# Performance work log

Measured on AMD Instinct MI355X. Metric: run time of the kernel, lower is better.

Reference implementation:

```python
import jax, jax.numpy as jnp
import numpy as np

EMBED = 1024
HEADS = 16
HEAD_DIM = EMBED // HEADS


def setup_inputs() -> dict:
    key = jax.random.key(0)
    ks = jax.random.split(key, 9)
    s = 1.0 / np.sqrt(EMBED)
    return {
        "x": jax.random.normal(ks[0], (4, 1024, EMBED), dtype=jnp.float32),
        "wq": jax.random.normal(ks[1], (EMBED, EMBED), dtype=jnp.float32) * s,
        "bq": jax.random.normal(ks[2], (EMBED,), dtype=jnp.float32) * s,
        "wk": jax.random.normal(ks[3], (EMBED, EMBED), dtype=jnp.float32) * s,
        "bk": jax.random.normal(ks[4], (EMBED,), dtype=jnp.float32) * s,
        "wv": jax.random.normal(ks[5], (EMBED, EMBED), dtype=jnp.float32) * s,
        "bv": jax.random.normal(ks[6], (EMBED,), dtype=jnp.float32) * s,
        "wo": jax.random.normal(ks[7], (EMBED, EMBED), dtype=jnp.float32) * s,
        "bo": jax.random.normal(ks[8], (EMBED,), dtype=jnp.float32) * s,
    }


def _split_heads(t):
    # (b, s, e) -> (b, h, s, d)
    b, s, _ = t.shape
    return t.reshape(b, s, HEADS, HEAD_DIM).transpose(0, 2, 1, 3)


def reference(x, wq, bq, wk, bk, wv, bv, wo, bo):
    # nn.Linear: y = x @ W.T + b
    q = _split_heads(x @ wq.T + bq)
    k = _split_heads(x @ wk.T + bk)
    v = _split_heads(x @ wv.T + bv)
    scale = 1.0 / jnp.sqrt(jnp.asarray(HEAD_DIM, dtype=x.dtype))
    scores = jnp.einsum("bhqd,bhkd->bhqk", q, k) * scale
    attn = jax.nn.softmax(scores, axis=-1)  # (b, h, s, s)
    ctx = jnp.einsum("bhqk,bhkd->bhqd", attn, v)
    b, h, s, d = ctx.shape
    ctx = ctx.transpose(0, 2, 1, 3).reshape(b, s, h * d)
    out = ctx @ wo.T + bo
    return out, attn
```

## Files before the change

kernel.cpp:

```cpp
#include <hip/hip_runtime.h>
#include <math.h>

#define BATCH 4
#define SEQ   1024
#define EMB   1024
#define HEADS 16
#define HD    64
#define MTOT  (BATCH*SEQ)

typedef float    f32x4 __attribute__((ext_vector_type(4)));
typedef float    vf4   __attribute__((ext_vector_type(4)));
typedef _Float16 f16;
typedef _Float16 f16x4 __attribute__((ext_vector_type(4)));
typedef _Float16 f16x8 __attribute__((ext_vector_type(8)));

__global__ __launch_bounds__(256) void convert_all(
    const float* __restrict__ x,
    const float* __restrict__ wq, const float* __restrict__ wk,
    const float* __restrict__ wv, const float* __restrict__ wo,
    f16* __restrict__ xh, f16* __restrict__ wh)
{
    const int bid = blockIdx.x;
    const float* src;
    f16* dst;
    if (bid < 4096) {
        src = x + ((size_t)bid << 10);
        dst = xh + ((size_t)bid << 10);
    } else {
        int t  = bid - 4096;
        int mi = t >> 10, r = t & 1023;
        const float* in = (mi == 0) ? wq : (mi == 1) ? wk : (mi == 2) ? wv : wo;
        src = in + ((size_t)r << 10);
        dst = wh + ((size_t)mi << 20) + ((size_t)r << 10);
    }
    int o = threadIdx.x << 2;
    float4 v = *(const float4*)(src + o);
    f16x4 h;
    h.x = (f16)v.x; h.y = (f16)v.y; h.z = (f16)v.z; h.w = (f16)v.w;
    *(f16x4*)(dst + o) = h;
}

#define BM  128
#define BN  128
#define LDT 72

__device__ __forceinline__ void mfma_gemm_tile(
    const f16* __restrict__ A, const f16* __restrict__ B,
    int m0, int n0, f32x4 acc[4][4])
{
    __shared__ f16 As[BM * LDT];
    __shared__ f16 Bs[BM * LDT];
    const int tid  = threadIdx.x;
    const int lane = tid & 63;
    const int w    = tid >> 6;
    const int wr   = w >> 1, wc = w & 1;
    const int fr   = lane & 15;
    const int kb   = lane >> 4;

#pragma unroll
    for (int i = 0; i < 4; ++i)
#pragma unroll
        for (int j = 0; j < 4; ++j) acc[i][j] = (f32x4){0.f, 0.f, 0.f, 0.f};

    f16x8 ra[4], rb[4];
#define LOAD_STEP(KT)                                                          \
    {                                                                          \
        int k0 = (KT) * 64;                                                    \
        _Pragma("unroll")                                                      \
        for (int i = 0; i < 4; ++i) {                                          \
            int c = tid + (i << 8);                                            \
            int row = c >> 3, cc = (c & 7) << 3;                               \
            ra[i] = *(const f16x8*)(A + ((size_t)(m0 + row) << 10) + k0 + cc); \
            rb[i] = *(const f16x8*)(B + ((size_t)(n0 + row) << 10) + k0 + cc); \
        }                                                                      \
    }

    LOAD_STEP(0);
    for (int kt = 0; kt < 16; ++kt) {
        __syncthreads();
#pragma unroll
        for (int i = 0; i < 4; ++i) {
            int c = tid + (i << 8);
            int row = c >> 3, cc = (c & 7) << 3;
            *(f16x8*)&As[row * LDT + cc] = ra[i];
            *(f16x8*)&Bs[row * LDT + cc] = rb[i];
        }
        if (kt + 1 < 16) LOAD_STEP(kt + 1);
        __syncthreads();
#pragma unroll
        for (int kc = 0; kc < 2; ++kc) {
            f16x8 aF[4], bF[4];
#pragma unroll
            for (int i = 0; i < 4; ++i)
                aF[i] = *(const f16x8*)&As[(wr * 64 + i * 16 + fr) * LDT + kc * 32 + kb * 8];
#pragma unroll
            for (int j = 0; j < 4; ++j)
                bF[j] = *(const f16x8*)&Bs[(wc * 64 + j * 16 + fr) * LDT + kc * 32 + kb * 8];
#pragma unroll
            for (int i = 0; i < 4; ++i)
#pragma unroll
                for (int j = 0; j < 4; ++j)
                    acc[i][j] = __builtin_amdgcn_mfma_f32_16x16x32_f16(
                        aF[i], bF[j], acc[i][j], 0, 0, 0);
        }
    }
#undef LOAD_STEP
}

__global__ __launch_bounds__(256, 2) void qkv_mfma(
    const f16* __restrict__ xh, const f16* __restrict__ wh,
    const float* __restrict__ bq, const float* __restrict__ bk,
    const float* __restrict__ bv,
    f16* __restrict__ qh, f16* __restrict__ kh, f16* __restrict__ vth)
{
    const int z = blockIdx.z;
    const f16* Bm = wh + ((size_t)z << 20);
    const float* bias = (z == 0) ? bq : (z == 1) ? bk : bv;
    const int m0 = blockIdx.y * BM, n0 = blockIdx.x * BN;
    f32x4 acc[4][4];
    mfma_gemm_tile(xh, Bm, m0, n0, acc);

    const int lane = threadIdx.x & 63;
    const int w    = threadIdx.x >> 6;
    const int wr   = w >> 1, wc = w & 1;
    const int fr   = lane & 15;
    const int rg   = lane >> 4;
#pragma unroll
    for (int i = 0; i < 4; ++i)
#pragma unroll
        for (int j = 0; j < 4; ++j) {
            int n = n0 + wc * 64 + j * 16 + fr;
            int h = n >> 6, d = n & 63;
            float bv_ = bias[n];
            int m_base = m0 + wr * 64 + i * 16 + rg * 4;
            int b = m_base >> 10, s0 = m_base & 1023;
            if (z < 2) {
                f16* p = (z == 0) ? qh : kh;
#pragma unroll
                for (int r = 0; r < 4; ++r) {
                    float v = acc[i][j][r] + bv_;
                    p[((size_t)((b * HEADS + h) * SEQ + s0 + r)) * HD + d] = (f16)v;
                }
            } else {
                f16x4 h4;
                h4.x = (f16)(acc[i][j][0] + bv_);
                h4.y = (f16)(acc[i][j][1] + bv_);
                h4.z = (f16)(acc[i][j][2] + bv_);
                h4.w = (f16)(acc[i][j][3] + bv_);
                size_t a = ((size_t)((b * HEADS + h) * HD + d)) * SEQ + s0;
                *(f16x4*)(vth + a) = h4;
            }
        }
}

__global__ __launch_bounds__(256, 2) void oproj_mfma(
    const f16* __restrict__ ch, const f16* __restrict__ wh,
    const float* __restrict__ bo, float* __restrict__ out)
{
    const f16* Bm = wh + ((size_t)3 << 20);
    const int m0 = blockIdx.y * BM, n0 = blockIdx.x * BN;
    f32x4 acc[4][4];
    mfma_gemm_tile(ch, Bm, m0, n0, acc);

    const int lane = threadIdx.x & 63;
    const int w    = threadIdx.x >> 6;
    const int wr   = w >> 1, wc = w & 1;
    const int fr   = lane & 15;
    const int rg   = lane >> 4;
#pragma unroll
    for (int i = 0; i < 4; ++i)
#pragma unroll
        for (int j = 0; j < 4; ++j) {
            int n = n0 + wc * 64 + j * 16 + fr;
            float bv_ = bo[n];
#pragma unroll
            for (int r = 0; r < 4; ++r) {
                int m = m0 + wr * 64 + i * 16 + rg * 4 + r;
                out[(size_t)m * EMB + n] = acc[i][j][r] + bv_;
            }
        }
}

__global__ __launch_bounds__(512, 4) void attn_kernel(
    const f16* __restrict__ qh, const f16* __restrict__ kh,
    const f16* __restrict__ vth,
    float* __restrict__ attn, f16* __restrict__ ch)
{
    __shared__ f16 SM[12288];
    __shared__ float RMAX[8][16];
    __shared__ float RSUM[8][16];

    const int lid = blockIdx.y * gridDim.x + blockIdx.x;
    const int xs  = lid & 7;
    const int jj  = lid >> 3;
    const int bh  = xs * 8 + (jj >> 5);
    const int qt  = jj & 31;

    const int tid  = threadIdx.x;
    const int w    = tid >> 6;
    const int grp  = w >> 2;
    const int wg   = w & 3;
    const int lane = tid & 63;
    const int c    = lane & 15;
    const int g    = lane >> 4;

    const size_t bhS = (size_t)bh * SEQ;

    f16x8 Q0, Q1;
    {
        size_t qb = (bhS + qt * 32 + grp * 16 + c) * HD + g * 8;
        Q0 = *(const f16x8*)(qh + qb);
        Q1 = *(const f16x8*)(qh + qb + 32);
    }

    f32x4 s4[16];
#pragma unroll
    for (int kt = 0; kt < 16; ++kt) s4[kt] = (f32x4){0.f, 0.f, 0.f, 0.f};

    const int srow = tid >> 3;
    const int sch  = tid & 7;
    const int sswz = sch ^ (srow & 7);
#pragma unroll
    for (int kt = 0; kt < 16; ++kt) {
        size_t ga = (bhS + kt * 64 + srow) * HD + sch * 8;
        f16x8 sh = *(const f16x8*)(kh + ga);
        __syncthreads();
        *(f16x8*)&SM[srow * 64 + sswz * 8] = sh;
        __syncthreads();
        const int krow = wg * 16 + c;
        const int cs   = c & 7;
        f16x8 B0 = *(const f16x8*)&SM[krow * 64 + ((0 + g) ^ cs) * 8];
        f16x8 B1 = *(const f16x8*)&SM[krow * 64 + ((4 + g) ^ cs) * 8];
        s4[kt] = __builtin_amdgcn_mfma_f32_16x16x32_f16(Q0, B0, s4[kt], 0, 0, 0);
        s4[kt] = __builtin_amdgcn_mfma_f32_16x16x32_f16(Q1, B1, s4[kt], 0, 0, 0);
    }

    float m_[4], l_[4];
#pragma unroll
    for (int r = 0; r < 4; ++r) {
        float mm = -1e30f;
#pragma unroll
        for (int kt = 0; kt < 16; ++kt) {
            s4[kt][r] *= 0.125f;
            mm = fmaxf(mm, s4[kt][r]);
        }
        m_[r] = mm;
    }
#pragma unroll
    for (int off = 1; off < 16; off <<= 1)
#pragma unroll
        for (int r = 0; r < 4; ++r) m_[r] = fmaxf(m_[r], __shfl_xor(m_[r], off));
    if (c == 0) {
#pragma unroll
        for (int r = 0; r < 4; ++r) RMAX[w][g * 4 + r] = m_[r];
    }
    __syncthreads();
#pragma unroll
    for (int r = 0; r < 4; ++r)
        m_[r] = fmaxf(fmaxf(RMAX[grp * 4 + 0][g * 4 + r], RMAX[grp * 4 + 1][g * 4 + r]),
                      fmaxf(RMAX[grp * 4 + 2][g * 4 + r], RMAX[grp * 4 + 3][g * 4 + r]));
#pragma unroll
    for (int r = 0; r < 4; ++r) {
        float ss = 0.f;
#pragma unroll
        for (int kt = 0; kt < 16; ++kt) {
            float p = __expf(s4[kt][r] - m_[r]);
            s4[kt][r] = p;
            ss += p;
        }
        l_[r] = ss;
    }
#pragma unroll
    for (int off = 1; off < 16; off <<= 1)
#pragma unroll
        for (int r = 0; r < 4; ++r) l_[r] += __shfl_xor(l_[r], off);
    if (c == 0) {
#pragma unroll
        for (int r = 0; r < 4; ++r) RSUM[w][g * 4 + r] = l_[r];
    }
    __syncthreads();
#pragma unroll
    for (int r = 0; r < 4; ++r)
        l_[r] = 1.f / (RSUM[grp * 4 + 0][g * 4 + r] + RSUM[grp * 4 + 1][g * 4 + r] +
                       RSUM[grp * 4 + 2][g * 4 + r] + RSUM[grp * 4 + 3][g * 4 + r]);

    f32x4 ctx = (f32x4){0.f, 0.f, 0.f, 0.f};
    float* ap = attn + (bhS + qt * 32) * SEQ;
    const int vrow0 = tid >> 4;
    const int vch   = tid & 15;

#pragma unroll
    for (int ct = 0; ct < 8; ++ct) {
        f16x8 vv[2];
#pragma unroll
        for (int t = 0; t < 2; ++t) {
            int drow = vrow0 + t * 32;
            size_t ga = ((size_t)bh * HD + drow) * SEQ + ct * 128 + vch * 8;
            vv[t] = *(const f16x8*)(vth + ga);
        }
        __syncthreads();
#pragma unroll
        for (int t = 0; t < 2; ++t) {
            int drow = vrow0 + t * 32;
            int swz = vch ^ (drow & 7);
            *(f16x8*)&SM[drow * 128 + swz * 8] = vv[t];
        }
#pragma unroll
        for (int kt2 = 0; kt2 < 2; ++kt2) {
            const int ktg = ct * 2 + kt2;
            const int chh = (kt2 * 64 + wg * 16 + c) >> 3;
#pragma unroll
            for (int r = 0; r < 4; ++r) {
                const int q = g * 4 + r;
                float val = s4[ktg][r] * l_[r];
                int schP = chh ^ q;
                SM[8192 + (grp * 16 + q) * 128 + schP * 8 + (c & 7)] = (f16)val;
            }
        }
        __syncthreads();
        const int drow = wg * 16 + c;
        const int ds7  = drow & 7;
#pragma unroll
        for (int ks = 0; ks < 4; ++ks) {
            f16x8 Vh = *(const f16x8*)&SM[drow * 128 + ((ks * 4 + g) ^ ds7) * 8];
            f16x8 Pa = *(const f16x8*)&SM[8192 + (grp * 16 + c) * 128 + (((ks * 4 + g) ^ c) & 15) * 8];
            ctx = __builtin_amdgcn_mfma_f32_16x16x32_f16(Pa, Vh, ctx, 0, 0, 0);
        }
#pragma unroll
        for (int t = 0; t < 2; ++t) {
            int idx = tid + (t << 9);
            int row = idx >> 5;
            int c4  = idx & 31;
            int col = c4 << 2;
            int swz = (col >> 3) ^ (row & 15);
            f16x4 pv = *(const f16x4*)&SM[8192 + row * 128 + swz * 8 + (col & 7)];
            vf4 o = __builtin_convertvector(pv, vf4);
            __builtin_nontemporal_store(o,
                (vf4*)(ap + (size_t)row * SEQ + ct * 128 + col));
        }
    }

    {
        int b = bh >> 4, h = bh & 15;
#pragma unroll
        for (int r = 0; r < 4; ++r) {
            int qrow = qt * 32 + grp * 16 + g * 4 + r;
            size_t a = (((size_t)(b * SEQ + qrow)) << 10) + h * HD + wg * 16 + c;
            ch[a] = (f16)ctx[r];
        }
    }
}

extern "C" void kernel_launch(void* const* d_in, const int* in_sizes, int n_in,
                              void* d_out, int out_size, void* d_ws, size_t ws_size,
                              hipStream_t stream) {
    const float* x  = (const float*)d_in[0];
    const float* wq = (const float*)d_in[1];
    const float* bq = (const float*)d_in[2];
    const float* wk = (const float*)d_in[3];
    const float* bk = (const float*)d_in[4];
    const float* wv = (const float*)d_in[5];
    const float* bv = (const float*)d_in[6];
    const float* wo = (const float*)d_in[7];
    const float* bo = (const float*)d_in[8];

    float* out      = (float*)d_out;
    float* attn_out = out + (size_t)BATCH * SEQ * EMB;

    const size_t MK = (size_t)MTOT * 1024;
    f16* ws16 = (f16*)d_ws;
    f16* xh  = ws16;
    f16* wh  = xh + MK;
    f16* qh  = wh + ((size_t)4 << 20);
    f16* kh  = qh + MK;
    f16* vth = kh + MK;
    f16* ch  = xh;

    convert_all<<<8192, 256, 0, stream>>>(x, wq, wk, wv, wo, xh, wh);

    qkv_mfma<<<dim3(EMB / BN, MTOT / BM, 3), 256, 0, stream>>>(
        xh, wh, bq, bk, bv, qh, kh, vth);

    attn_kernel<<<dim3(SEQ / 32, BATCH * HEADS), 512, 0, stream>>>(
        qh, kh, vth, attn_out, ch);

    oproj_mfma<<<dim3(EMB / BN, MTOT / BM), 256, 0, stream>>>(
        ch, wh, bo, out);
}
```

Before: 148.2 us.

## Stage GEMM epilogues through LDS and prefetch K/V tiles in attention

The QKV and output-projection GEMM epilogues now write through shared memory so global stores go out as coalesced 16-byte vectors, replacing scattered 2-byte and 4-byte stores. This includes the transposed V layout. The attention kernel loads K in 128-row chunks and prefetches the next K and V tile into registers while the current tile is staged and consumed. This hides global load latency and halves the barrier pairs in the QK loop. In exchange it adds extra LDS round trips and barriers in the epilogues and raises register pressure in the attention kernel.

After: 138.1 us. -6.8%, faster.

```diff
diff --git a/kernel.cpp b/kernel.cpp
--- a/kernel.cpp
+++ b/kernel.cpp
@@ -46,10 +46,10 @@
 
 __device__ __forceinline__ void mfma_gemm_tile(
     const f16* __restrict__ A, const f16* __restrict__ B,
-    int m0, int n0, f32x4 acc[4][4])
+    int m0, int n0, f32x4 acc[4][4], f16* SMEM)
 {
-    __shared__ f16 As[BM * LDT];
-    __shared__ f16 Bs[BM * LDT];
+    f16* As = SMEM;
+    f16* Bs = SMEM + BM * LDT;
     const int tid  = threadIdx.x;
     const int lane = tid & 63;
     const int w    = tid >> 6;
@@ -113,72 +113,118 @@
     const float* __restrict__ bv,
     f16* __restrict__ qh, f16* __restrict__ kh, f16* __restrict__ vth)
 {
+    __shared__ __align__(16) f16 SMEM[2 * BM * LDT];
     const int z = blockIdx.z;
     const f16* Bm = wh + ((size_t)z << 20);
     const float* bias = (z == 0) ? bq : (z == 1) ? bk : bv;
     const int m0 = blockIdx.y * BM, n0 = blockIdx.x * BN;
     f32x4 acc[4][4];
-    mfma_gemm_tile(xh, Bm, m0, n0, acc);
-
-    const int lane = threadIdx.x & 63;
-    const int w    = threadIdx.x >> 6;
+    mfma_gemm_tile(xh, Bm, m0, n0, acc, SMEM);
+
+    const int tid  = threadIdx.x;
+    const int lane = tid & 63;
+    const int w    = tid >> 6;
     const int wr   = w >> 1, wc = w & 1;
     const int fr   = lane & 15;
     const int rg   = lane >> 4;
-#pragma unroll
-    for (int i = 0; i < 4; ++i)
-#pragma unroll
-        for (int j = 0; j < 4; ++j) {
-            int n = n0 + wc * 64 + j * 16 + fr;
-            int h = n >> 6, d = n & 63;
-            float bv_ = bias[n];
-            int m_base = m0 + wr * 64 + i * 16 + rg * 4;
-            int b = m_base >> 10, s0 = m_base & 1023;
-            if (z < 2) {
-                f16* p = (z == 0) ? qh : kh;
+    const int LDC  = 136;
+    const int b = m0 >> 10, sbase = m0 & 1023;
+
+    __syncthreads();
+    if (z < 2) {
+        f16* p = (z == 0) ? qh : kh;
+#pragma unroll
+        for (int i = 0; i < 4; ++i)
+#pragma unroll
+            for (int j = 0; j < 4; ++j) {
+                int nn = wc * 64 + j * 16 + fr;
+                float bv_ = bias[n0 + nn];
 #pragma unroll
                 for (int r = 0; r < 4; ++r) {
-                    float v = acc[i][j][r] + bv_;
-                    p[((size_t)((b * HEADS + h) * SEQ + s0 + r)) * HD + d] = (f16)v;
+                    int mm = wr * 64 + i * 16 + rg * 4 + r;
+                    SMEM[mm * LDC + nn] = (f16)(acc[i][j][r] + bv_);
                 }
-            } else {
-                f16x4 h4;
-                h4.x = (f16)(acc[i][j][0] + bv_);
-                h4.y = (f16)(acc[i][j][1] + bv_);
-                h4.z = (f16)(acc[i][j][2] + bv_);
-                h4.w = (f16)(acc[i][j][3] + bv_);
-                size_t a = ((size_t)((b * HEADS + h) * HD + d)) * SEQ + s0;
-                *(f16x4*)(vth + a) = h4;
             }
-        }
+        __syncthreads();
+#pragma unroll
+        for (int t = 0; t < 8; ++t) {
+            int idx = tid + (t << 8);
+            int row = idx >> 4, ch = idx & 15;
+            int n8 = n0 + ch * 8;
+            int h = n8 >> 6, d = n8 & 63;
+            f16x8 v = *(const f16x8*)&SMEM[row * LDC + ch * 8];
+            *(f16x8*)(p + ((size_t)((b * HEADS + h) * SEQ + sbase + row)) * HD + d) = v;
+        }
+    } else {
+#pragma unroll
+        for (int i = 0; i < 4; ++i)
+#pragma unroll
+            for (int j = 0; j < 4; ++j) {
+                int nn = wc * 64 + j * 16 + fr;
+                float bv_ = bias[n0 + nn];
+#pragma unroll
+                for (int r = 0; r < 4; ++r) {
+                    int mm = wr * 64 + i * 16 + rg * 4 + r;
+                    SMEM[nn * LDC + mm] = (f16)(acc[i][j][r] + bv_);
+                }
+            }
+        __syncthreads();
+#pragma unroll
+        for (int t = 0; t < 8; ++t) {
+            int idx = tid + (t << 8);
+            int col = idx >> 4, mch = idx & 15;
+            int n8 = n0 + col;
+            int h = n8 >> 6, d = n8 & 63;
+            f16x8 v = *(const f16x8*)&SMEM[col * LDC + mch * 8];
+            *(f16x8*)(vth + ((size_t)((b * HEADS + h) * HD + d)) * SEQ + sbase + mch * 8) = v;
+        }
+    }
 }
 
 __global__ __launch_bounds__(256, 2) void oproj_mfma(
     const f16* __restrict__ ch, const f16* __restrict__ wh,
     const float* __restrict__ bo, float* __restrict__ out)
 {
+    __shared__ __align__(16) f16 SMEM[2 * BM * LDT];
     const f16* Bm = wh + ((size_t)3 << 20);
     const int m0 = blockIdx.y * BM, n0 = blockIdx.x * BN;
     f32x4 acc[4][4];
-    mfma_gemm_tile(ch, Bm, m0, n0, acc);
-
-    const int lane = threadIdx.x & 63;
-    const int w    = threadIdx.x >> 6;
+    mfma_gemm_tile(ch, Bm, m0, n0, acc, SMEM);
+
+    const int tid  = threadIdx.x;
+    const int lane = tid & 63;
+    const int w    = tid >> 6;
     const int wr   = w >> 1, wc = w & 1;
     const int fr   = lane & 15;
     const int rg   = lane >> 4;
-#pragma unroll
-    for (int i = 0; i < 4; ++i)
-#pragma unroll
-        for (int j = 0; j < 4; ++j) {
-            int n = n0 + wc * 64 + j * 16 + fr;
-            float bv_ = bo[n];
-#pragma unroll
-            for (int r = 0; r < 4; ++r) {
-                int m = m0 + wr * 64 + i * 16 + rg * 4 + r;
-                out[(size_t)m * EMB + n] = acc[i][j][r] + bv_;
-            }
-        }
+    float* Cf = (float*)SMEM;
+    const int LDCf = 132;
+
+#pragma unroll
+    for (int half = 0; half < 2; ++half) {
+        __syncthreads();
+        if (wr == half) {
+#pragma unroll
+            for (int i = 0; i < 4; ++i)
+#pragma unroll
+                for (int j = 0; j < 4; ++j) {
+                    int nn = wc * 64 + j * 16 + fr;
+                    float bv_ = bo[n0 + nn];
+#pragma unroll
+                    for (int r = 0; r < 4; ++r)
+                        Cf[(i * 16 + rg * 4 + r) * LDCf + nn] = acc[i][j][r] + bv_;
+                }
+        }
+        __syncthreads();
+#pragma unroll
+        for (int t = 0; t < 8; ++t) {
+            int idx = tid + (t << 8);
+            int row = idx >> 5, c4 = (idx & 31) << 2;
+            vf4 v = *(const vf4*)&Cf[row * LDCf + c4];
+            __builtin_nontemporal_store(v,
+                (vf4*)(out + (size_t)(m0 + half * 64 + row) * EMB + n0 + c4));
+        }
+    }
 }
 
 __global__ __launch_bounds__(512, 4) void attn_kernel(
@@ -219,20 +265,38 @@
 
     const int srow = tid >> 3;
     const int sch  = tid & 7;
-    const int sswz = sch ^ (srow & 7);
-#pragma unroll
-    for (int kt = 0; kt < 16; ++kt) {
-        size_t ga = (bhS + kt * 64 + srow) * HD + sch * 8;
-        f16x8 sh = *(const f16x8*)(kh + ga);
-        __syncthreads();
-        *(f16x8*)&SM[srow * 64 + sswz * 8] = sh;
-        __syncthreads();
-        const int krow = wg * 16 + c;
-        const int cs   = c & 7;
-        f16x8 B0 = *(const f16x8*)&SM[krow * 64 + ((0 + g) ^ cs) * 8];
-        f16x8 B1 = *(const f16x8*)&SM[krow * 64 + ((4 + g) ^ cs) * 8];
-        s4[kt] = __builtin_amdgcn_mfma_f32_16x16x32_f16(Q0, B0, s4[kt], 0, 0, 0);
-        s4[kt] = __builtin_amdgcn_mfma_f32_16x16x32_f16(Q1, B1, s4[kt], 0, 0, 0);
+    f16x8 kc0, kc1, kn0, kn1;
+    {
+        size_t ga = (bhS + srow) * HD + sch * 8;
+        kc0 = *(const f16x8*)(kh + ga);
+        kc1 = *(const f16x8*)(kh + ga + (size_t)64 * HD);
+    }
+#pragma unroll
+    for (int kt2 = 0; kt2 < 8; ++kt2) {
+        __syncthreads();
+        {
+            int r1 = srow + 64;
+            *(f16x8*)&SM[srow * 64 + (sch ^ (srow & 7)) * 8] = kc0;
+            *(f16x8*)&SM[r1 * 64 + (sch ^ (r1 & 7)) * 8]     = kc1;
+        }
+        if (kt2 < 7) {
+            size_t ga = (bhS + (kt2 + 1) * 128 + srow) * HD + sch * 8;
+            kn0 = *(const f16x8*)(kh + ga);
+            kn1 = *(const f16x8*)(kh + ga + (size_t)64 * HD);
+        }
+        __syncthreads();
+#pragma unroll
+        for (int half = 0; half < 2; ++half) {
+            const int krow = half * 64 + wg * 16 + c;
+            const int ks7  = krow & 7;
+            f16x8 B0 = *(const f16x8*)&SM[krow * 64 + ((0 + g) ^ ks7) * 8];
+            f16x8 B1 = *(const f16x8*)&SM[krow * 64 + ((4 + g) ^ ks7) * 8];
+            s4[kt2 * 2 + half] = __builtin_amdgcn_mfma_f32_16x16x32_f16(
+                Q0, B0, s4[kt2 * 2 + half], 0, 0, 0);
+            s4[kt2 * 2 + half] = __builtin_amdgcn_mfma_f32_16x16x32_f16(
+                Q1, B1, s4[kt2 * 2 + half], 0, 0, 0);
+        }
+        kc0 = kn0; kc1 = kn1;
     }
 
     float m_[4], l_[4];
@@ -289,21 +353,28 @@
     const int vrow0 = tid >> 4;
     const int vch   = tid & 15;
 
+    f16x8 vc[2], vn[2];
+#pragma unroll
+    for (int t = 0; t < 2; ++t) {
+        int drow = vrow0 + t * 32;
+        vc[t] = *(const f16x8*)(vth + ((size_t)bh * HD + drow) * SEQ + vch * 8);
+    }
 #pragma unroll
     for (int ct = 0; ct < 8; ++ct) {
-        f16x8 vv[2];
-#pragma unroll
-        for (int t = 0; t < 2; ++t) {
-            int drow = vrow0 + t * 32;
-            size_t ga = ((size_t)bh * HD + drow) * SEQ + ct * 128 + vch * 8;
-            vv[t] = *(const f16x8*)(vth + ga);
-        }
         __syncthreads();
 #pragma unroll
         for (int t = 0; t < 2; ++t) {
             int drow = vrow0 + t * 32;
             int swz = vch ^ (drow & 7);
-            *(f16x8*)&SM[drow * 128 + swz * 8] = vv[t];
+            *(f16x8*)&SM[drow * 128 + swz * 8] = vc[t];
+        }
+        if (ct < 7) {
+#pragma unroll
+            for (int t = 0; t < 2; ++t) {
+                int drow = vrow0 + t * 32;
+                vn[t] = *(const f16x8*)(vth + ((size_t)bh * HD + drow) * SEQ +
+                                        (ct + 1) * 128 + vch * 8);
+            }
         }
 #pragma unroll
         for (int kt2 = 0; kt2 < 2; ++kt2) {
@@ -338,6 +409,7 @@
             __builtin_nontemporal_store(o,
                 (vf4*)(ap + (size_t)row * SEQ + ct * 128 + col));
         }
+        vc[0] = vn[0]; vc[1] = vn[1];
     }
 
     {
```
